# Kernel optimization log

Hardware: AMD Instinct MI355X
Metric: run time of the kernel (lower is better)

## Reference

```python
import jax, jax.numpy as jnp
import numpy as np

NUM_BLOCKS = 32
B, S = 8, 2048


def setup_inputs() -> dict:
    key = jax.random.key(0)
    k1, k2, k3 = jax.random.split(key, 3)
    h = jax.random.uniform(k1, (B, S, NUM_BLOCKS, 4), dtype=jnp.float32)
    W = jax.random.uniform(k2, (B, S, NUM_BLOCKS, NUM_BLOCKS), dtype=jnp.float32)
    stim = jax.random.uniform(k3, (B, S, NUM_BLOCKS), dtype=jnp.float32)
    return {"h": h, "W": W, "stim": stim}


def _step(h, W, stim):
    nb = h.shape[-2]
    eye = jnp.eye(nb, dtype=W.dtype)
    W_no_self = W * (1.0 - eye)                      # zero self-connections
    # neighbor inflow: [b,s,i,j] @ [b,s,j,c] -> [b,s,i,c]
    inflow = jnp.einsum('bsij,bsjc->bsic', W_no_self, h)
    total_w = W_no_self.sum(axis=-1, keepdims=True) + 1e-8
    neigh = inflow / total_w                          # weighted neighbor mean

    E, P, G, L = h[..., 0], h[..., 1], h[..., 2], h[..., 3]
    En, Pn, Gn, Ln = neigh[..., 0], neigh[..., 1], neigh[..., 2], neigh[..., 3]

    clamp01 = lambda x: jnp.clip(x, 0.0, 1.0)
    E_new = clamp01(E + 0.3 * stim - 0.4 * P - 0.2 * G)
    P_new = clamp01(P + 0.5 * stim + 0.3 * (Pn - P) - 0.2 * E)
    G_new = clamp01(G + 0.4 * E * (1.0 - P) + 0.2 * (Gn - G) - 0.3 * P)
    good_neighbor = 0.5 * En + 0.5 * Gn
    L_new = clamp01(L + 0.4 * good_neighbor + 0.3 * (Ln - L) - 0.3 * P)

    h_new = jnp.stack([E_new, P_new, G_new, L_new], axis=-1)  # [b,s,nb,4]

    # pairwise euclidean distance over the 4 EPGL channels (torch.cdist p=2)
    diff = h_new[..., :, None, :] - h_new[..., None, :, :]    # [b,s,nb,nb,4]
    sq = jnp.sum(diff * diff, axis=-1)
    # safe sqrt: zero distance -> 0 (matches cdist; avoids nan grads)
    h_diff = jnp.where(sq > 0, jnp.sqrt(jnp.where(sq > 0, sq, 1.0)), 0.0)

    mutual_L = 0.5 * (L_new[..., :, None] + L_new[..., None, :])
    alpha, beta = 0.1 * mutual_L, 0.05
    W_new = W + alpha * h_diff - beta * W
    W_new = jnp.clip(W_new, 0.0, 1.0) * (1.0 - eye)
    return h_new, W_new


def reference(h, W, stim):
    return _step(h, W, stim)
```

## Files before the change

### kernel.cpp

```cpp
#include <hip/hip_runtime.h>

#define NB 32
#define WAVES_PER_BLOCK 4

__device__ __forceinline__ float clamp01(float x) {
    return fminf(fmaxf(x, 0.0f), 1.0f);
}

__global__ __launch_bounds__(256, 8) void biotoken_step(
    const float* __restrict__ h,
    const float* __restrict__ W,
    const float* __restrict__ stim,
    float* __restrict__ out_h,
    float* __restrict__ out_W)
{
    const int lw    = threadIdx.x & 63;
    const int wave  = threadIdx.x >> 6;
    const int token = blockIdx.x * WAVES_PER_BLOCK + wave;

    __shared__ float s_hin [WAVES_PER_BLOCK][NB * 4];
    __shared__ float s_W   [WAVES_PER_BLOCK][NB * 33];

    const float4* Wt = (const float4*)(W + (size_t)token * (NB * NB));
    const float4* ht = (const float4*)(h + (size_t)token * (NB * 4));

    float4 wr[4];
    wr[0] = Wt[0 * 64 + lw];
    wr[1] = Wt[1 * 64 + lw];
    wr[2] = Wt[2 * 64 + lw];
    wr[3] = Wt[3 * 64 + lw];

    const int i    = lw & 31;
    const int half = lw >> 5;
    const float sti = stim[(size_t)token * NB + i];

    if (lw < NB) {
        ((float4*)s_hin[wave])[lw] = ht[lw];
    }

    {
        float* sw = s_W[wave];
        const int g = lw >> 3;
        const int c = (lw & 7) * 4;
        #pragma unroll
        for (int k = 0; k < 4; ++k) {
            const int r = k * 8 + g;
            const float* wp = (const float*)&wr[k];
            sw[r * 33 + c + 0] = wp[0];
            sw[r * 33 + c + 1] = wp[1];
            sw[r * 33 + c + 2] = wp[2];
            sw[r * 33 + c + 3] = wp[3];
        }
    }
    __syncthreads();

    const float* sw   = s_W[wave];
    const float* shin = s_hin[wave];

    float accE = 0.f, accP = 0.f, accG = 0.f, accL = 0.f, tot = 0.f;
    #pragma unroll
    for (int t = 0; t < 16; ++t) {
        const int j = half * 16 + t;
        float w = sw[i * 33 + j];
        w = (j == i) ? 0.0f : w;
        const float4 hj = *(const float4*)&shin[j * 4];
        accE = fmaf(w, hj.x, accE);
        accP = fmaf(w, hj.y, accP);
        accG = fmaf(w, hj.z, accG);
        accL = fmaf(w, hj.w, accL);
        tot += w;
    }
    accE += __shfl_xor(accE, 32);
    accP += __shfl_xor(accP, 32);
    accG += __shfl_xor(accG, 32);
    accL += __shfl_xor(accL, 32);
    tot  += __shfl_xor(tot,  32);

    const float inv = 1.0f / (tot + 1e-8f);
    const float En = accE * inv, Pn = accP * inv, Gn = accG * inv, Ln = accL * inv;

    const float4 hi = *(const float4*)&shin[i * 4];
    const float E = hi.x, P = hi.y, G = hi.z, L = hi.w;

    const float E_new = clamp01(E + 0.3f * sti - 0.4f * P - 0.2f * G);
    const float P_new = clamp01(P + 0.5f * sti + 0.3f * (Pn - P) - 0.2f * E);
    const float G_new = clamp01(G + 0.4f * E * (1.0f - P) + 0.2f * (Gn - G) - 0.3f * P);
    const float good  = 0.5f * En + 0.5f * Gn;
    const float L_new = clamp01(L + 0.4f * good + 0.3f * (Ln - L) - 0.3f * P);

    if (half == 0) {
        const float4 hn = make_float4(E_new, P_new, G_new, L_new);
        ((float4*)s_W[wave])[i] = hn;
        ((float4*)(out_h + (size_t)token * (NB * 4)))[i] = hn;
    }
    __syncthreads();

    const float* shn = s_W[wave];
    float4* outWt = (float4*)(out_W + (size_t)token * (NB * NB));

    const int jb0 = (lw & 7) * 4;
    float4 hjv[4];
    #pragma unroll
    for (int e = 0; e < 4; ++e) {
        hjv[e] = *(const float4*)&shn[(jb0 + e) * 4];
    }

    #pragma unroll
    for (int k = 0; k < 4; ++k) {
        const int m  = k * 64 + lw;
        const int r  = m >> 3;
        const float4 hr = *(const float4*)&shn[r * 4];
        const float  Lr = hr.w;
        const float* wp = (const float*)&wr[k];
        float4 res;
        float* resp = &res.x;
        #pragma unroll
        for (int e = 0; e < 4; ++e) {
            const int j = jb0 + e;
            const float4 hj = hjv[e];
            const float dx = hr.x - hj.x;
            const float dy = hr.y - hj.y;
            const float dz = hr.z - hj.z;
            const float dw = hr.w - hj.w;
            const float sq = dx * dx + dy * dy + dz * dz + dw * dw;
            const float dist = sqrtf(sq);
            const float mutual = 0.5f * (Lr + hj.w);
            float wn = 0.95f * wp[e] + 0.1f * mutual * dist;
            wn = clamp01(wn);
            resp[e] = (j == r) ? 0.0f : wn;
        }
        outWt[m] = res;
    }
}

extern "C" void kernel_launch(void* const* d_in, const int* in_sizes, int n_in,
                              void* d_out, int out_size, void* d_ws, size_t ws_size,
                              hipStream_t stream) {
    const float* h    = (const float*)d_in[0];
    const float* W    = (const float*)d_in[1];
    const float* stim = (const float*)d_in[2];

    const int tokens = in_sizes[2] / NB;
    float* out_h = (float*)d_out;
    float* out_W = (float*)d_out + (size_t)tokens * NB * 4;

    const int blocks = tokens / WAVES_PER_BLOCK;
    biotoken_step<<<blocks, 256, 0, stream>>>(h, W, stim, out_h, out_W);
}
```

Measured before the change: 135.5 us.

## Process two tokens per wave with both W tiles prefetched up front

Each wave now handles two consecutive tokens. It issues the global loads for both 4 KB W tiles before any compute starts, so the second token's load latency overlaps the first token's work. The block-wide __syncthreads calls after the first setup are replaced with wave barriers, because each wave only touches its own shared-memory slice. The cost is more live registers, and launch bounds drop from 8 to 6 blocks per SM. The grid is also halved, which lowers available parallelism and the number of waves in flight.

```diff
diff --git a/kernel.cpp b/kernel.cpp
--- a/kernel.cpp
+++ b/kernel.cpp
@@ -7,61 +7,36 @@
     return fminf(fmaxf(x, 0.0f), 1.0f);
 }
 
-__global__ __launch_bounds__(256, 8) void biotoken_step(
-    const float* __restrict__ h,
-    const float* __restrict__ W,
-    const float* __restrict__ stim,
-    float* __restrict__ out_h,
-    float* __restrict__ out_W)
+__device__ __forceinline__ void scatter_W(float* sw, const float4* wr, int lw) {
+    const int g = lw >> 3;
+    const int c = (lw & 7) * 4;
+    #pragma unroll
+    for (int k = 0; k < 4; ++k) {
+        const int r = k * 8 + g;
+        const float* wp = (const float*)&wr[k];
+        sw[r * 33 + c + 0] = wp[0];
+        sw[r * 33 + c + 1] = wp[1];
+        sw[r * 33 + c + 2] = wp[2];
+        sw[r * 33 + c + 3] = wp[3];
+    }
+}
+
+__device__ __forceinline__ void process_token(
+    const float* __restrict__ shin,
+    float*       swave,
+    const float4* wr,
+    float sti, int lw,
+    float* __restrict__ out_h_t,
+    float4* __restrict__ outWt)
 {
-    const int lw    = threadIdx.x & 63;
-    const int wave  = threadIdx.x >> 6;
-    const int token = blockIdx.x * WAVES_PER_BLOCK + wave;
-
-    __shared__ float s_hin [WAVES_PER_BLOCK][NB * 4];
-    __shared__ float s_W   [WAVES_PER_BLOCK][NB * 33];
-
-    const float4* Wt = (const float4*)(W + (size_t)token * (NB * NB));
-    const float4* ht = (const float4*)(h + (size_t)token * (NB * 4));
-
-    float4 wr[4];
-    wr[0] = Wt[0 * 64 + lw];
-    wr[1] = Wt[1 * 64 + lw];
-    wr[2] = Wt[2 * 64 + lw];
-    wr[3] = Wt[3 * 64 + lw];
-
     const int i    = lw & 31;
     const int half = lw >> 5;
-    const float sti = stim[(size_t)token * NB + i];
-
-    if (lw < NB) {
-        ((float4*)s_hin[wave])[lw] = ht[lw];
-    }
-
-    {
-        float* sw = s_W[wave];
-        const int g = lw >> 3;
-        const int c = (lw & 7) * 4;
-        #pragma unroll
-        for (int k = 0; k < 4; ++k) {
-            const int r = k * 8 + g;
-            const float* wp = (const float*)&wr[k];
-            sw[r * 33 + c + 0] = wp[0];
-            sw[r * 33 + c + 1] = wp[1];
-            sw[r * 33 + c + 2] = wp[2];
-            sw[r * 33 + c + 3] = wp[3];
-        }
-    }
-    __syncthreads();
-
-    const float* sw   = s_W[wave];
-    const float* shin = s_hin[wave];
 
     float accE = 0.f, accP = 0.f, accG = 0.f, accL = 0.f, tot = 0.f;
     #pragma unroll
     for (int t = 0; t < 16; ++t) {
         const int j = half * 16 + t;
-        float w = sw[i * 33 + j];
+        float w = swave[i * 33 + j];
         w = (j == i) ? 0.0f : w;
         const float4 hj = *(const float4*)&shin[j * 4];
         accE = fmaf(w, hj.x, accE);
@@ -90,14 +65,12 @@
 
     if (half == 0) {
         const float4 hn = make_float4(E_new, P_new, G_new, L_new);
-        ((float4*)s_W[wave])[i] = hn;
-        ((float4*)(out_h + (size_t)token * (NB * 4)))[i] = hn;
+        ((float4*)swave)[i] = hn;
+        ((float4*)out_h_t)[i] = hn;
     }
-    __syncthreads();
+    __builtin_amdgcn_wave_barrier();
 
-    const float* shn = s_W[wave];
-    float4* outWt = (float4*)(out_W + (size_t)token * (NB * NB));
-
+    const float* shn = swave;
     const int jb0 = (lw & 7) * 4;
     float4 hjv[4];
     #pragma unroll
@@ -133,6 +106,55 @@
     }
 }
 
+__global__ __launch_bounds__(256, 6) void biotoken_step(
+    const float* __restrict__ h,
+    const float* __restrict__ W,
+    const float* __restrict__ stim,
+    float* __restrict__ out_h,
+    float* __restrict__ out_W)
+{
+    const int lw   = threadIdx.x & 63;
+    const int wave = threadIdx.x >> 6;
+    const int tokA = (blockIdx.x * WAVES_PER_BLOCK + wave) * 2;
+    const int i    = lw & 31;
+
+    __shared__ float s_hin[WAVES_PER_BLOCK][2][NB * 4];
+    __shared__ float s_W  [WAVES_PER_BLOCK][NB * 33];
+
+    const float4* WtA = (const float4*)(W + (size_t)tokA * (NB * NB));
+    float4 wA[4], wB[4];
+    wA[0] = WtA[0 * 64 + lw];
+    wA[1] = WtA[1 * 64 + lw];
+    wA[2] = WtA[2 * 64 + lw];
+    wA[3] = WtA[3 * 64 + lw];
+    wB[0] = WtA[256 + 0 * 64 + lw];
+    wB[1] = WtA[256 + 1 * 64 + lw];
+    wB[2] = WtA[256 + 2 * 64 + lw];
+    wB[3] = WtA[256 + 3 * 64 + lw];
+
+    {
+        const int buf = lw >> 5;
+        ((float4*)s_hin[wave][buf])[i] =
+            ((const float4*)(h + (size_t)(tokA + buf) * (NB * 4)))[i];
+    }
+    const float stiA = stim[(size_t)tokA * NB + i];
+    const float stiB = stim[(size_t)(tokA + 1) * NB + i];
+
+    scatter_W(s_W[wave], wA, lw);
+    __syncthreads();
+
+    process_token(s_hin[wave][0], s_W[wave], wA, stiA, lw,
+                  out_h + (size_t)tokA * (NB * 4),
+                  (float4*)(out_W + (size_t)tokA * (NB * NB)));
+
+    __builtin_amdgcn_wave_barrier();
+    scatter_W(s_W[wave], wB, lw);
+    __builtin_amdgcn_wave_barrier();
+    process_token(s_hin[wave][1], s_W[wave], wB, stiB, lw,
+                  out_h + (size_t)(tokA + 1) * (NB * 4),
+                  (float4*)(out_W + (size_t)(tokA + 1) * (NB * NB)));
+}
+
 extern "C" void kernel_launch(void* const* d_in, const int* in_sizes, int n_in,
                               void* d_out, int out_size, void* d_ws, size_t ws_size,
                               hipStream_t stream) {
@@ -144,6 +166,6 @@
     float* out_h = (float*)d_out;
     float* out_W = (float*)d_out + (size_t)tokens * NB * 4;
 
-    const int blocks = tokens / WAVES_PER_BLOCK;
+    const int blocks = tokens / (WAVES_PER_BLOCK * 2);
     biotoken_step<<<blocks, 256, 0, stream>>>(h, W, stim, out_h, out_W);
 }
```

Result: slower. 160.1 us (+18.2%).
